# Kernel optimization log

Hardware: AMD Instinct MI355X
Metric: run time of the kernel (lower is better)

The kernel has to match this reference:

```python
import jax, jax.numpy as jnp
import numpy as np

B = 4096      # number of query nodes (len(samp_neighs))
U = 50000     # number of unique sampled neighbor nodes
D = 300       # node feature dim (GloVe-style ConceptNet embeddings)
E = 131072    # total (node, neighbor) pairs, avg degree ~32


def setup_inputs() -> dict:
    key = jax.random.key(0)
    k1, k2, k3 = jax.random.split(key, 3)
    row_idx = jnp.sort(jax.random.randint(k1, (E,), 0, B, dtype=jnp.int64 if jax.config.jax_enable_x64 else jnp.int32)).astype(jnp.int32)
    col_idx = jax.random.randint(k2, (E,), 0, U).astype(jnp.int32)
    embed_matrix = jax.random.normal(k3, (U, D), dtype=jnp.float32)
    return {"row_idx": row_idx, "col_idx": col_idx, "embed_matrix": embed_matrix}


def reference(row_idx, col_idx, embed_matrix):
    # Build dense neighbor-membership mask [B, U]; .set (not .add) mirrors the
    # original's set semantics (duplicate neighbors count once).
    mask = jnp.zeros((B, U), dtype=embed_matrix.dtype).at[row_idx, col_idx].set(1.0)
    num_neigh = mask.sum(axis=1, keepdims=True)            # [B, 1]
    mask = mask / jnp.clip(num_neigh, 1e-8)                # row-normalize (mean)
    to_feats = mask @ embed_matrix                         # [B, D] mean aggregation
    return to_feats
```

## Files before the change

### kernel.cpp

```cpp
#include <hip/hip_runtime.h>


#define DFEAT  300
#define NCHUNK 75
#define CAP    128
#define WPB    4

__global__ __launch_bounds__(256) void build_rowptr(
    const int* __restrict__ row_idx, int E, int B, int* __restrict__ row_ptr)
{
    const int e = blockIdx.x * 256 + threadIdx.x;
    if (e >= E) return;
    const int r     = row_idx[e];
    const int rprev = (e == 0) ? -1 : row_idx[e - 1];
    for (int x = rprev + 1; x <= r; ++x) row_ptr[x] = e;
    if (e == E - 1) {
        for (int x = r + 1; x <= B; ++x) row_ptr[x] = E;
    }
}

__global__ __launch_bounds__(256) void mean_agg_kernel(
    const int* __restrict__ row_ptr,
    const int* __restrict__ col_idx,
    const float* __restrict__ embed,
    float* __restrict__ out,
    int B)
{
    const int lane = threadIdx.x & 63;
    const int w    = threadIdx.x >> 6;
    const int b    = blockIdx.x * WPB + w;
    if (b >= B) return;

    __shared__ int s_uniq[WPB][CAP];

    const int start = row_ptr[b];
    const int deg   = row_ptr[b + 1] - start;

    int cnt = 0;
    for (int base = 0; base < deg; base += 64) {
        const int  i     = base + lane;
        const bool valid = (i < deg);
        const int  c     = valid ? col_idx[start + i] : -1;

        bool dup = false;
        for (int q = 0; q < cnt; ++q) dup = dup || (s_uniq[w][q] == c);
        const int jmax = (deg - base - 1 < 63) ? (deg - base - 1) : 63;
        for (int j = 0; j < jmax; ++j) {
            const int cj = __shfl(c, j);
            dup = dup || ((j < lane) && (cj == c));
        }

        const unsigned long long m = __ballot(valid && !dup);
        const int rank = __popcll(m & ((1ull << lane) - 1ull));
        if (valid && !dup) {
            const int p = cnt + rank;
            if (p < CAP) s_uniq[w][p] = c;
        }
        cnt += (int)__popcll(m);
    }
    if (cnt > CAP) cnt = CAP;

    const bool hi = (lane < NCHUNK - 64);
    float4 a0 = {0.f, 0.f, 0.f, 0.f};
    float4 a1 = {0.f, 0.f, 0.f, 0.f};

    int u = 0;
    for (; u + 4 <= cnt; u += 4) {
        const float4* __restrict__ p0 = (const float4*)(embed + (size_t)s_uniq[w][u    ] * DFEAT);
        const float4* __restrict__ p1 = (const float4*)(embed + (size_t)s_uniq[w][u + 1] * DFEAT);
        const float4* __restrict__ p2 = (const float4*)(embed + (size_t)s_uniq[w][u + 2] * DFEAT);
        const float4* __restrict__ p3 = (const float4*)(embed + (size_t)s_uniq[w][u + 3] * DFEAT);
        const float4 v0 = p0[lane];
        const float4 v1 = p1[lane];
        const float4 v2 = p2[lane];
        const float4 v3 = p3[lane];
        if (hi) {
            const float4 h0 = p0[lane + 64];
            const float4 h1 = p1[lane + 64];
            const float4 h2 = p2[lane + 64];
            const float4 h3 = p3[lane + 64];
            a1.x += h0.x + h1.x + h2.x + h3.x;
            a1.y += h0.y + h1.y + h2.y + h3.y;
            a1.z += h0.z + h1.z + h2.z + h3.z;
            a1.w += h0.w + h1.w + h2.w + h3.w;
        }
        a0.x += v0.x + v1.x + v2.x + v3.x;
        a0.y += v0.y + v1.y + v2.y + v3.y;
        a0.z += v0.z + v1.z + v2.z + v3.z;
        a0.w += v0.w + v1.w + v2.w + v3.w;
    }
    for (; u < cnt; ++u) {
        const float4* __restrict__ p0 = (const float4*)(embed + (size_t)s_uniq[w][u] * DFEAT);
        const float4 v0 = p0[lane];
        a0.x += v0.x; a0.y += v0.y; a0.z += v0.z; a0.w += v0.w;
        if (hi) {
            const float4 h0 = p0[lane + 64];
            a1.x += h0.x; a1.y += h0.y; a1.z += h0.z; a1.w += h0.w;
        }
    }

    const float s = (cnt > 0) ? (1.0f / (float)cnt) : 0.0f;
    float4* __restrict__ orow = (float4*)(out + (size_t)b * DFEAT);
    float4 r0; r0.x = a0.x * s; r0.y = a0.y * s; r0.z = a0.z * s; r0.w = a0.w * s;
    orow[lane] = r0;
    if (hi) {
        float4 r1; r1.x = a1.x * s; r1.y = a1.y * s; r1.z = a1.z * s; r1.w = a1.w * s;
        orow[lane + 64] = r1;
    }
}

extern "C" void kernel_launch(void* const* d_in, const int* in_sizes, int n_in,
                              void* d_out, int out_size, void* d_ws, size_t ws_size,
                              hipStream_t stream) {
    const int*   row_idx = (const int*)  d_in[0];
    const int*   col_idx = (const int*)  d_in[1];
    const float* embed   = (const float*)d_in[2];
    float*       out     = (float*)      d_out;

    const int E = in_sizes[0];
    const int B = out_size / DFEAT;

    int* row_ptr = (int*)d_ws;

    build_rowptr<<<(E + 255) / 256, 256, 0, stream>>>(row_idx, E, B, row_ptr);
    mean_agg_kernel<<<(B + WPB - 1) / WPB, 256, 0, stream>>>(row_ptr, col_idx, embed, out, B);
}
```

Measured before the change: 110.3 us.

## Split each row across two wavefronts with prefetched neighbor indices

Each output row is now handled by a 128-thread block of two wavefronts that split the 75 float4 feature chunks (38 and 37). This replaces the single wavefront per row whose 11-lane tail needed a second predicated load. Both wavefronts repeat the dedup scan, and the gather loop reads the next four neighbor indices from shared memory while the current loads are in flight. Addressing uses 32-bit byte offsets, and launch bounds of 128 threads with 8 blocks ask for higher occupancy. The cost is the doubled dedup work and partly idle lanes in both wavefronts.

Measured after the change: 110.6 us. Within noise of the previous version (+0.3%).

```diff
diff --git a/kernel.cpp b/kernel.cpp
--- a/kernel.cpp
+++ b/kernel.cpp
@@ -4,7 +4,6 @@
 #define DFEAT  300
 #define NCHUNK 75
 #define CAP    128
-#define WPB    4
 
 __global__ __launch_bounds__(256) void build_rowptr(
     const int* __restrict__ row_idx, int E, int B, int* __restrict__ row_ptr)
@@ -19,7 +18,7 @@
     }
 }
 
-__global__ __launch_bounds__(256) void mean_agg_kernel(
+__global__ __launch_bounds__(128, 8) void mean_agg_kernel(
     const int* __restrict__ row_ptr,
     const int* __restrict__ col_idx,
     const float* __restrict__ embed,
@@ -28,10 +27,10 @@
 {
     const int lane = threadIdx.x & 63;
     const int w    = threadIdx.x >> 6;
-    const int b    = blockIdx.x * WPB + w;
+    const int b    = blockIdx.x;
     if (b >= B) return;
 
-    __shared__ int s_uniq[WPB][CAP];
+    __shared__ int s_uniq[2][CAP];
 
     const int start = row_ptr[b];
     const int deg   = row_ptr[b + 1] - start;
@@ -60,52 +59,56 @@
     }
     if (cnt > CAP) cnt = CAP;
 
-    const bool hi = (lane < NCHUNK - 64);
-    float4 a0 = {0.f, 0.f, 0.f, 0.f};
-    float4 a1 = {0.f, 0.f, 0.f, 0.f};
+    const int nact = w ? (NCHUNK - 38) : 38;
+    const int ch   = lane + w * 38;
+    if (lane < nact) {
+        const uint32_t off = (uint32_t)ch * 16u;
+        const char* __restrict__ eb = (const char*)embed;
 
-    int u = 0;
-    for (; u + 4 <= cnt; u += 4) {
-        const float4* __restrict__ p0 = (const float4*)(embed + (size_t)s_uniq[w][u    ] * DFEAT);
-        const float4* __restrict__ p1 = (const float4*)(embed + (size_t)s_uniq[w][u + 1] * DFEAT);
-        const float4* __restrict__ p2 = (const float4*)(embed + (size_t)s_uniq[w][u + 2] * DFEAT);
-        const float4* __restrict__ p3 = (const float4*)(embed + (size_t)s_uniq[w][u + 3] * DFEAT);
-        const float4 v0 = p0[lane];
-        const float4 v1 = p1[lane];
-        const float4 v2 = p2[lane];
-        const float4 v3 = p3[lane];
-        if (hi) {
-            const float4 h0 = p0[lane + 64];
-            const float4 h1 = p1[lane + 64];
-            const float4 h2 = p2[lane + 64];
-            const float4 h3 = p3[lane + 64];
-            a1.x += h0.x + h1.x + h2.x + h3.x;
-            a1.y += h0.y + h1.y + h2.y + h3.y;
-            a1.z += h0.z + h1.z + h2.z + h3.z;
-            a1.w += h0.w + h1.w + h2.w + h3.w;
+        float4 acc = {0.f, 0.f, 0.f, 0.f};
+
+        int u = 0;
+        int c0 = 0, c1 = 0, c2 = 0, c3 = 0;
+        if (cnt >= 4) {
+            c0 = s_uniq[w][0]; c1 = s_uniq[w][1];
+            c2 = s_uniq[w][2]; c3 = s_uniq[w][3];
         }
-        a0.x += v0.x + v1.x + v2.x + v3.x;
-        a0.y += v0.y + v1.y + v2.y + v3.y;
-        a0.z += v0.z + v1.z + v2.z + v3.z;
-        a0.w += v0.w + v1.w + v2.w + v3.w;
-    }
-    for (; u < cnt; ++u) {
-        const float4* __restrict__ p0 = (const float4*)(embed + (size_t)s_uniq[w][u] * DFEAT);
-        const float4 v0 = p0[lane];
-        a0.x += v0.x; a0.y += v0.y; a0.z += v0.z; a0.w += v0.w;
-        if (hi) {
-            const float4 h0 = p0[lane + 64];
-            a1.x += h0.x; a1.y += h0.y; a1.z += h0.z; a1.w += h0.w;
+        for (; u + 8 <= cnt; u += 4) {
+            const float4 v0 = *(const float4*)(eb + ((uint32_t)c0 * 1200u + off));
+            const float4 v1 = *(const float4*)(eb + ((uint32_t)c1 * 1200u + off));
+            const float4 v2 = *(const float4*)(eb + ((uint32_t)c2 * 1200u + off));
+            const float4 v3 = *(const float4*)(eb + ((uint32_t)c3 * 1200u + off));
+            const int n0 = s_uniq[w][u + 4];
+            const int n1 = s_uniq[w][u + 5];
+            const int n2 = s_uniq[w][u + 6];
+            const int n3 = s_uniq[w][u + 7];
+            acc.x += v0.x + v1.x + v2.x + v3.x;
+            acc.y += v0.y + v1.y + v2.y + v3.y;
+            acc.z += v0.z + v1.z + v2.z + v3.z;
+            acc.w += v0.w + v1.w + v2.w + v3.w;
+            c0 = n0; c1 = n1; c2 = n2; c3 = n3;
         }
-    }
+        if (u + 4 <= cnt) {
+            const float4 v0 = *(const float4*)(eb + ((uint32_t)c0 * 1200u + off));
+            const float4 v1 = *(const float4*)(eb + ((uint32_t)c1 * 1200u + off));
+            const float4 v2 = *(const float4*)(eb + ((uint32_t)c2 * 1200u + off));
+            const float4 v3 = *(const float4*)(eb + ((uint32_t)c3 * 1200u + off));
+            acc.x += v0.x + v1.x + v2.x + v3.x;
+            acc.y += v0.y + v1.y + v2.y + v3.y;
+            acc.z += v0.z + v1.z + v2.z + v3.z;
+            acc.w += v0.w + v1.w + v2.w + v3.w;
+            u += 4;
+        }
+        for (; u < cnt; ++u) {
+            const int cS = s_uniq[w][u];
+            const float4 v = *(const float4*)(eb + ((uint32_t)cS * 1200u + off));
+            acc.x += v.x; acc.y += v.y; acc.z += v.z; acc.w += v.w;
+        }
 
-    const float s = (cnt > 0) ? (1.0f / (float)cnt) : 0.0f;
-    float4* __restrict__ orow = (float4*)(out + (size_t)b * DFEAT);
-    float4 r0; r0.x = a0.x * s; r0.y = a0.y * s; r0.z = a0.z * s; r0.w = a0.w * s;
-    orow[lane] = r0;
-    if (hi) {
-        float4 r1; r1.x = a1.x * s; r1.y = a1.y * s; r1.z = a1.z * s; r1.w = a1.w * s;
-        orow[lane + 64] = r1;
+        const float s = (cnt > 0) ? (1.0f / (float)cnt) : 0.0f;
+        float4 r;
+        r.x = acc.x * s; r.y = acc.y * s; r.z = acc.z * s; r.w = acc.w * s;
+        *(float4*)((char*)out + (size_t)b * 1200u + (uint32_t)ch * 16u) = r;
     }
 }
 
@@ -123,5 +126,5 @@
     int* row_ptr = (int*)d_ws;
 
     build_rowptr<<<(E + 255) / 256, 256, 0, stream>>>(row_idx, E, B, row_ptr);
-    mean_agg_kernel<<<(B + WPB - 1) / WPB, 256, 0, stream>>>(row_ptr, col_idx, embed, out, B);
+    mean_agg_kernel<<<B, 128, 0, stream>>>(row_ptr, col_idx, embed, out, B);
 }
```

## Fuse row-pointer build into aggregation via per-wave binary search

Applied to the files above, without the earlier changes.

Drops the separate row_ptr construction kernel. Each wave now finds its row start in the sorted row_idx with a 64-way parallel binary search. For rows with fewer than 64 entries it loads all columns in one pass, sums every column, and then subtracts the duplicate rows instead of compacting a unique list. This saves a kernel launch and the workspace round trip, at the cost of extra search loads per wave and re-fetching the duplicate embedding rows.

Measured after the change: 111.0 us. No clear change (+0.6%).

```diff
diff --git a/kernel.cpp b/kernel.cpp
--- a/kernel.cpp
+++ b/kernel.cpp
@@ -6,70 +6,103 @@
 #define CAP    128
 #define WPB    4
 
-__global__ __launch_bounds__(256) void build_rowptr(
-    const int* __restrict__ row_idx, int E, int B, int* __restrict__ row_ptr)
+__device__ __forceinline__ int wave_lower_bound(
+    const int* __restrict__ arr, int E, int t, int lane)
 {
-    const int e = blockIdx.x * 256 + threadIdx.x;
-    if (e >= E) return;
-    const int r     = row_idx[e];
-    const int rprev = (e == 0) ? -1 : row_idx[e - 1];
-    for (int x = rprev + 1; x <= r; ++x) row_ptr[x] = e;
-    if (e == E - 1) {
-        for (int x = r + 1; x <= B; ++x) row_ptr[x] = E;
+    int lo = 0, hi = E;
+    while (hi - lo > 64) {
+        const int span = hi - lo;
+        const int p    = lo + (int)(((long long)span * (long long)lane) >> 6);
+        const int v    = arr[p];
+        const unsigned long long m = __ballot(v < t);
+        if (m == 0) return lo;
+        const int k   = 63 - __clzll(m);
+        const int pk  = __shfl(p, k);
+        const int pk1 = __shfl(p, (k + 1) & 63);
+        lo = pk + 1;
+        if (k < 63) hi = pk1;
     }
+    const int p = lo + lane;
+    const int v = (p < hi) ? arr[p] : 0x7fffffff;
+    const unsigned long long m = __ballot(v < t);
+    return lo + (int)__popcll(m);
 }
 
-__global__ __launch_bounds__(256) void mean_agg_kernel(
-    const int* __restrict__ row_ptr,
+__global__ __launch_bounds__(256) void mean_agg_fused(
+    const int* __restrict__ row_idx,
     const int* __restrict__ col_idx,
     const float* __restrict__ embed,
     float* __restrict__ out,
-    int B)
+    int E, int B)
 {
     const int lane = threadIdx.x & 63;
     const int w    = threadIdx.x >> 6;
     const int b    = blockIdx.x * WPB + w;
     if (b >= B) return;
 
-    __shared__ int s_uniq[WPB][CAP];
+    __shared__ int s_cols[WPB][CAP];
 
-    const int start = row_ptr[b];
-    const int deg   = row_ptr[b + 1] - start;
+    const int start = wave_lower_bound(row_idx, E, b, lane);
 
-    int cnt = 0;
-    for (int base = 0; base < deg; base += 64) {
-        const int  i     = base + lane;
-        const bool valid = (i < deg);
-        const int  c     = valid ? col_idx[start + i] : -1;
+    const int  i0    = start + lane;
+    const bool inE   = (i0 < E);
+    const int  rv    = inE ? row_idx[i0] : 0x7fffffff;
+    const int  c0raw = inE ? col_idx[i0] : -1;
+    const unsigned long long mrow = __ballot(rv == b);
+    const int deg0 = (int)__popcll(mrow);
 
+    int n;
+    int cnt;
+    unsigned long long mdup = 0;
+
+    if (deg0 < 64) {
+        n = deg0;
+        s_cols[w][lane] = c0raw;
         bool dup = false;
-        for (int q = 0; q < cnt; ++q) dup = dup || (s_uniq[w][q] == c);
-        const int jmax = (deg - base - 1 < 63) ? (deg - base - 1) : 63;
-        for (int j = 0; j < jmax; ++j) {
-            const int cj = __shfl(c, j);
-            dup = dup || ((j < lane) && (cj == c));
+        for (int j = 0; j < deg0 - 1; ++j) {
+            const int cj = __shfl(c0raw, j);
+            dup = dup || ((j < lane) && (cj == c0raw));
         }
-
-        const unsigned long long m = __ballot(valid && !dup);
-        const int rank = __popcll(m & ((1ull << lane) - 1ull));
-        if (valid && !dup) {
-            const int p = cnt + rank;
-            if (p < CAP) s_uniq[w][p] = c;
+        dup  = dup && (lane < deg0);
+        mdup = __ballot(dup);
+        cnt  = deg0 - (int)__popcll(mdup);
+    } else {
+        const int end = wave_lower_bound(row_idx, E, b + 1, lane);
+        const int deg = end - start;
+        cnt = 0;
+        for (int base = 0; base < deg; base += 64) {
+            const int  i     = base + lane;
+            const bool valid = (i < deg);
+            const int  c     = valid ? col_idx[start + i] : -1;
+            bool dup = false;
+            for (int q = 0; q < cnt; ++q) dup = dup || (s_cols[w][q] == c);
+            const int jmax = (deg - base - 1 < 63) ? (deg - base - 1) : 63;
+            for (int j = 0; j < jmax; ++j) {
+                const int cj = __shfl(c, j);
+                dup = dup || ((j < lane) && (cj == c));
+            }
+            const unsigned long long m = __ballot(valid && !dup);
+            const int rank = (int)__popcll(m & ((1ull << lane) - 1ull));
+            if (valid && !dup) {
+                const int p = cnt + rank;
+                if (p < CAP) s_cols[w][p] = c;
+            }
+            cnt += (int)__popcll(m);
         }
-        cnt += (int)__popcll(m);
+        if (cnt > CAP) cnt = CAP;
+        n = cnt;
     }
-    if (cnt > CAP) cnt = CAP;
 
     const bool hi = (lane < NCHUNK - 64);
     float4 a0 = {0.f, 0.f, 0.f, 0.f};
     float4 a1 = {0.f, 0.f, 0.f, 0.f};
 
     int u = 0;
-    for (; u + 4 <= cnt; u += 4) {
-        const float4* __restrict__ p0 = (const float4*)(embed + (size_t)s_uniq[w][u    ] * DFEAT);
-        const float4* __restrict__ p1 = (const float4*)(embed + (size_t)s_uniq[w][u + 1] * DFEAT);
-        const float4* __restrict__ p2 = (const float4*)(embed + (size_t)s_uniq[w][u + 2] * DFEAT);
-        const float4* __restrict__ p3 = (const float4*)(embed + (size_t)s_uniq[w][u + 3] * DFEAT);
+    for (; u + 4 <= n; u += 4) {
+        const float4* __restrict__ p0 = (const float4*)(embed + (size_t)s_cols[w][u    ] * DFEAT);
+        const float4* __restrict__ p1 = (const float4*)(embed + (size_t)s_cols[w][u + 1] * DFEAT);
+        const float4* __restrict__ p2 = (const float4*)(embed + (size_t)s_cols[w][u + 2] * DFEAT);
+        const float4* __restrict__ p3 = (const float4*)(embed + (size_t)s_cols[w][u + 3] * DFEAT);
         const float4 v0 = p0[lane];
         const float4 v1 = p1[lane];
         const float4 v2 = p2[lane];
@@ -89,13 +122,29 @@
         a0.z += v0.z + v1.z + v2.z + v3.z;
         a0.w += v0.w + v1.w + v2.w + v3.w;
     }
-    for (; u < cnt; ++u) {
-        const float4* __restrict__ p0 = (const float4*)(embed + (size_t)s_uniq[w][u] * DFEAT);
+    for (; u < n; ++u) {
+        const float4* __restrict__ p0 = (const float4*)(embed + (size_t)s_cols[w][u] * DFEAT);
         const float4 v0 = p0[lane];
         a0.x += v0.x; a0.y += v0.y; a0.z += v0.z; a0.w += v0.w;
         if (hi) {
             const float4 h0 = p0[lane + 64];
             a1.x += h0.x; a1.y += h0.y; a1.z += h0.z; a1.w += h0.w;
+        }
+    }
+
+    if (mdup) {
+        unsigned long long m = mdup;
+        while (m) {
+            const int d = (int)__builtin_ctzll(m);
+            m &= m - 1;
+            const int cd = s_cols[w][d];
+            const float4* __restrict__ p = (const float4*)(embed + (size_t)cd * DFEAT);
+            const float4 v = p[lane];
+            a0.x -= v.x; a0.y -= v.y; a0.z -= v.z; a0.w -= v.w;
+            if (hi) {
+                const float4 h = p[lane + 64];
+                a1.x -= h.x; a1.y -= h.y; a1.z -= h.z; a1.w -= h.w;
+            }
         }
     }
 
@@ -120,8 +169,6 @@
     const int E = in_sizes[0];
     const int B = out_size / DFEAT;
 
-    int* row_ptr = (int*)d_ws;
-
-    build_rowptr<<<(E + 255) / 256, 256, 0, stream>>>(row_idx, E, B, row_ptr);
-    mean_agg_kernel<<<(B + WPB - 1) / WPB, 256, 0, stream>>>(row_ptr, col_idx, embed, out, B);
+    mean_agg_fused<<<(B + WPB - 1) / WPB, 256, 0, stream>>>(
+        row_idx, col_idx, embed, out, E, B);
 }
```
